# Performance work log

Measured on AMD Instinct MI355X. Metric: run time of the kernel, lower is better.

Reference implementation:

```python
import jax, jax.numpy as jnp
import numpy as np

S, N, IN = 4096, 32, 4
H, IF, SF, OUT = 64, 8, 4, 2
N_PAIRS = N * (N - 1)


def setup_inputs() -> dict:
    key = jax.random.key(0)
    ks = jax.random.split(key, 12)
    f = jax.random.normal
    return {
        "inputs": f(ks[0], (S, N, IN), jnp.float32),
        "L1W": f(ks[1], (H, IN), jnp.float32) * 0.1,
        "L1b": f(ks[2], (H,), jnp.float32) * 0.1,
        "L2W": f(ks[3], (H, H), jnp.float32) * 0.1,
        "L2b": f(ks[4], (H,), jnp.float32) * 0.1,
        "I1W": f(ks[5], (H, H), jnp.float32) * 0.1,
        "I2W": f(ks[6], (IF, H), jnp.float32) * 0.1,
        "I3": f(ks[7], (N_PAIRS, OUT, IF // OUT), jnp.float32) * 0.01,
        "S1W": f(ks[8], (SF, IN), jnp.float32) * 0.1,
        "S1b": f(ks[9], (SF,), jnp.float32) * 0.1,
        "S2W": f(ks[10], (N, OUT, SF // OUT), jnp.float32) * 0.01,
        "S2b": jnp.zeros((N, OUT), jnp.float32),
    }


def reference(inputs, L1W, L1b, L2W, L2b, I1W, I2W, I3, S1W, S1b, S2W, S2b):
    seq_len, n_obj = inputs.shape[:2]
    out_size = S2b.shape[1]

    # shared encoders (torch Linear: x @ W.T + b)
    h = jax.nn.relu(inputs @ L1W.T + L1b)
    h = jax.nn.relu(h @ L2W.T + L2b)          # [S, N, H]
    hs = jax.nn.relu(inputs @ S1W.T + S1b)    # [S, N, SF]

    # all pairwise differences Xi - Xj -> edge MLP (no biases)
    diff = h[:, :, None, :] - h[:, None, :, :]      # [S, N, N, H]
    pair = jnp.tanh(diff @ I1W.T)                   # [S, N, N, H]
    pair = jnp.tanh(pair @ I2W.T)                   # [S, N, N, IF]
    k_int = pair.shape[-1] // out_size
    pair = pair.reshape(seq_len, n_obj, n_obj, out_size, k_int)

    # scatter per-pair weights I3 into dense [N, N, OUT, k] using the
    # row-major Table ordering (i, j != i); diagonal stays zero, which
    # matches the original since diag pairwise features are exactly 0.
    ii, jj = np.nonzero(~np.eye(n_obj, dtype=bool))
    I3d = jnp.zeros((n_obj, n_obj, out_size, k_int), I3.dtype).at[ii, jj].set(I3)

    interaction = jnp.einsum('sijdk,ijdk->sid', pair, I3d)  # [S, N, OUT]

    k_self = hs.shape[-1] // out_size
    hs = hs.reshape(seq_len, n_obj, out_size, k_self)
    self_term = jnp.einsum('sidk,idk->sid', hs, S2W) + S2b  # [S, N, OUT]

    return interaction + self_term
```

## Files before the change

kernel.cpp:

```cpp
#include <hip/hip_runtime.h>
#include <math.h>

#define SEQ   4096
#define NOBJ  32
#define IN_F  4
#define HID   64
#define IFEAT 8
#define NPAIR_HALF 496

#define TWO_LOG2E 2.8853900817779268f

#if __has_builtin(__builtin_amdgcn_exp2f)
  #define EXP2F(x) __builtin_amdgcn_exp2f(x)
#else
  #define EXP2F(x) exp2f(x)
#endif

typedef _Float16 h2    __attribute__((ext_vector_type(2)));
typedef _Float16 f16x8 __attribute__((ext_vector_type(8)));
typedef float    f32x4 __attribute__((ext_vector_type(4)));

__device__ __forceinline__ h2 pack2(float a, float b) {
  return __builtin_bit_cast(h2, __builtin_amdgcn_cvt_pkrtz(a, b));
}
__device__ __forceinline__ unsigned pbits(h2 v) { return __builtin_bit_cast(unsigned, v); }

__device__ __forceinline__ f16x8 pack8(float4 a, float4 b) {
  int4 v;
  v.x = (int)pbits(pack2(a.x, a.y));
  v.y = (int)pbits(pack2(a.z, a.w));
  v.z = (int)pbits(pack2(b.x, b.y));
  v.w = (int)pbits(pack2(b.z, b.w));
  return __builtin_bit_cast(f16x8, v);
}

__device__ __forceinline__ float tanh_u(float x) {
  float e = EXP2F(x * TWO_LOG2E);
  float r = __builtin_amdgcn_rcpf(e + 1.0f);
  return fmaf(-2.0f, r, 1.0f);
}

__device__ __forceinline__ int pair_cum(int i) { return (i * (63 - i)) >> 1; }

__device__ __forceinline__ void pair_decode(int q, int& i, int& j) {
  int ii = (int)((63.0f - sqrtf(3969.0f - 8.0f * (float)q)) * 0.5f);
  if (ii > 0 && pair_cum(ii) > q) --ii;
  if (pair_cum(ii + 1) <= q)     ++ii;
  i = ii;
  j = ii + 1 + (q - pair_cum(ii));
}

__global__ __launch_bounds__(256, 4) void magnet_fused(
    const float* __restrict__ x,
    const float* __restrict__ L1W,
    const float* __restrict__ L1b,
    const float* __restrict__ L2W,
    const float* __restrict__ L2b,
    const float* __restrict__ I1W,
    const float* __restrict__ I2W,
    const float* __restrict__ I3,
    const float* __restrict__ S1W,
    const float* __restrict__ S1b,
    const float* __restrict__ S2W,
    const float* __restrict__ S2b,
    float* __restrict__ out)
{
  __shared__ __align__(16) float smem[6824];
  unsigned* sAtp   = (unsigned*)smem;
  unsigned* sBtp   = (unsigned*)(smem + 1152);
  float*    pairval = smem;
  float*    sE  = smem + 2304;
  float*    sEm = smem + 4480;
  float*    sx  = smem + 6656;
  float*    sW  = smem + 6784;

  const int t = threadIdx.x;
  const int s = blockIdx.x;

  if (t < NOBJ * IN_F) sx[t] = x[s * (NOBJ * IN_F) + t];
  if (t < IFEAT) {
    float a = 0.0f;
    const float4* w = (const float4*)(I2W + t * HID);
    #pragma unroll
    for (int c = 0; c < 16; ++c) { float4 v = w[c]; a += (v.x + v.y) + (v.z + v.w); }
    sW[t] = a;
  }
  __syncthreads();

  {
    const int n = t & 31, gI = t >> 5, kb = gI * 8;
    const float x0 = sx[n * 4 + 0], x1 = sx[n * 4 + 1];
    const float x2 = sx[n * 4 + 2], x3 = sx[n * 4 + 3];
    float a[8];
    #pragma unroll
    for (int r = 0; r < 8; ++r) {
      const int k = kb + r;
      const float4 w = *(const float4*)(L1W + k * 4);
      float v = L1b[k];
      v = fmaf(x0, w.x, v); v = fmaf(x1, w.y, v);
      v = fmaf(x2, w.z, v); v = fmaf(x3, w.w, v);
      a[r] = fmaxf(v, 0.0f);
    }
    int4 pk;
    pk.x = (int)pbits(pack2(a[0], a[1]));
    pk.y = (int)pbits(pack2(a[2], a[3]));
    pk.z = (int)pbits(pack2(a[4], a[5]));
    pk.w = (int)pbits(pack2(a[6], a[7]));
    *(int4*)(sAtp + n * 36 + gI * 4) = pk;
  }
  __syncthreads();

  const int lane = t & 63;
  const int wv   = t >> 6;
  const int qd   = lane >> 4;
  const int ln   = lane & 15;

  {
    const int m = 16 * wv + ln;
    const float* wr = L2W + m * HID;
    const f16x8 A0 = pack8(*(const float4*)(wr + 8 * qd),
                           *(const float4*)(wr + 8 * qd + 4));
    const f16x8 A1 = pack8(*(const float4*)(wr + 32 + 8 * qd),
                           *(const float4*)(wr + 32 + 8 * qd + 4));
    const float4 bias = *(const float4*)(L2b + 16 * wv + 4 * qd);
    #pragma unroll
    for (int nt = 0; nt < 2; ++nt) {
      const int n = nt * 16 + ln;
      const f16x8 B0 = __builtin_bit_cast(f16x8, *(const int4*)(sAtp + n * 36 + 4 * qd));
      const f16x8 B1 = __builtin_bit_cast(f16x8, *(const int4*)(sAtp + n * 36 + 16 + 4 * qd));
      f32x4 c; c[0] = bias.x; c[1] = bias.y; c[2] = bias.z; c[3] = bias.w;
      c = __builtin_amdgcn_mfma_f32_16x16x32_f16(A0, B0, c, 0, 0, 0);
      c = __builtin_amdgcn_mfma_f32_16x16x32_f16(A1, B1, c, 0, 0, 0);
      sBtp[n * 36 + 8 * wv + 2 * qd]     = pbits(pack2(fmaxf(c[0], 0.f), fmaxf(c[1], 0.f)));
      sBtp[n * 36 + 8 * wv + 2 * qd + 1] = pbits(pack2(fmaxf(c[2], 0.f), fmaxf(c[3], 0.f)));
    }
  }
  __syncthreads();

  {
    const int m = 16 * wv + ln;
    const float* wr = I1W + m * HID;
    const f16x8 A0 = pack8(*(const float4*)(wr + 8 * qd),
                           *(const float4*)(wr + 8 * qd + 4));
    const f16x8 A1 = pack8(*(const float4*)(wr + 32 + 8 * qd),
                           *(const float4*)(wr + 32 + 8 * qd + 4));
    #pragma unroll
    for (int nt = 0; nt < 2; ++nt) {
      const int n = nt * 16 + ln;
      const f16x8 B0 = __builtin_bit_cast(f16x8, *(const int4*)(sBtp + n * 36 + 4 * qd));
      const f16x8 B1 = __builtin_bit_cast(f16x8, *(const int4*)(sBtp + n * 36 + 16 + 4 * qd));
      f32x4 c; c[0] = 0.f; c[1] = 0.f; c[2] = 0.f; c[3] = 0.f;
      c = __builtin_amdgcn_mfma_f32_16x16x32_f16(A0, B0, c, 0, 0, 0);
      c = __builtin_amdgcn_mfma_f32_16x16x32_f16(A1, B1, c, 0, 0, 0);
      #pragma unroll
      for (int r = 0; r < 4; ++r) {
        const int mo = 16 * wv + 4 * qd + r;
        float gp = fminf(fmaxf(c[r] * TWO_LOG2E, -60.0f), 60.0f);
        sE [n * 68 + mo] = EXP2F(gp);
        sEm[n * 68 + mo] = EXP2F(-gp);
      }
    }
  }
  __syncthreads();

  {
    int i1, j1, i2, j2;
    pair_decode(t, i1, j1);
    const bool has2 = (t + 256) < NPAIR_HALF;
    pair_decode(has2 ? t + 256 : 0, i2, j2);

    float sWr[IFEAT];
    #pragma unroll
    for (int f = 0; f < IFEAT; ++f) sWr[f] = sW[f];

    float da[IFEAT] = {0.f,0.f,0.f,0.f,0.f,0.f,0.f,0.f};
    float db[IFEAT] = {0.f,0.f,0.f,0.f,0.f,0.f,0.f,0.f};
    const float4* Ei1 = (const float4*)(sE  + i1 * 68);
    const float4* Mj1 = (const float4*)(sEm + j1 * 68);
    const float4* Ei2 = (const float4*)(sE  + i2 * 68);
    const float4* Mj2 = (const float4*)(sEm + j2 * 68);

    #pragma unroll 4
    for (int hb = 0; hb < 16; ++hb) {
      const float4 a1 = Ei1[hb], b1 = Mj1[hb];
      const float4 a2 = Ei2[hb], b2 = Mj2[hb];
      float r1[4], r2[4];
      #pragma unroll
      for (int c = 0; c < 4; ++c) {
        r1[c] = __builtin_amdgcn_rcpf(fmaf((&a1.x)[c], (&b1.x)[c], 1.0f));
        r2[c] = __builtin_amdgcn_rcpf(fmaf((&a2.x)[c], (&b2.x)[c], 1.0f));
      }
      #pragma unroll
      for (int f = 0; f < IFEAT; ++f) {
        const float4 w = *(const float4*)(I2W + f * HID + hb * 4);
        da[f] = fmaf(w.x, r1[0], da[f]); da[f] = fmaf(w.y, r1[1], da[f]);
        da[f] = fmaf(w.z, r1[2], da[f]); da[f] = fmaf(w.w, r1[3], da[f]);
        db[f] = fmaf(w.x, r2[0], db[f]); db[f] = fmaf(w.y, r2[1], db[f]);
        db[f] = fmaf(w.z, r2[2], db[f]); db[f] = fmaf(w.w, r2[3], db[f]);
      }
    }

    {
      const float* cij = I3 + (i1 * 31 + (j1 - 1)) * 8;
      const float* cji = I3 + (j1 * 31 + i1) * 8;
      float vi0 = 0.f, vi1 = 0.f, vj0 = 0.f, vj1 = 0.f;
      #pragma unroll
      for (int k = 0; k < 4; ++k) {
        const float v = tanh_u(fmaf(-2.0f, da[k], sWr[k]));
        vi0 = fmaf(cij[k],  v, vi0);
        vj0 = fmaf(cji[k], -v, vj0);
      }
      #pragma unroll
      for (int k = 0; k < 4; ++k) {
        const float v = tanh_u(fmaf(-2.0f, da[4 + k], sWr[4 + k]));
        vi1 = fmaf(cij[4 + k],  v, vi1);
        vj1 = fmaf(cji[4 + k], -v, vj1);
      }
      float4 pv; pv.x = vi0; pv.y = vi1; pv.z = vj0; pv.w = vj1;
      *(float4*)(pairval + t * 4) = pv;
    }
    if (has2) {
      const float* cij = I3 + (i2 * 31 + (j2 - 1)) * 8;
      const float* cji = I3 + (j2 * 31 + i2) * 8;
      float vi0 = 0.f, vi1 = 0.f, vj0 = 0.f, vj1 = 0.f;
      #pragma unroll
      for (int k = 0; k < 4; ++k) {
        const float v = tanh_u(fmaf(-2.0f, db[k], sWr[k]));
        vi0 = fmaf(cij[k],  v, vi0);
        vj0 = fmaf(cji[k], -v, vj0);
      }
      #pragma unroll
      for (int k = 0; k < 4; ++k) {
        const float v = tanh_u(fmaf(-2.0f, db[4 + k], sWr[4 + k]));
        vi1 = fmaf(cij[4 + k],  v, vi1);
        vj1 = fmaf(cji[4 + k], -v, vj1);
      }
      float4 pv; pv.x = vi0; pv.y = vi1; pv.z = vj0; pv.w = vj1;
      *(float4*)(pairval + (t + 256) * 4) = pv;
    }
  }
  __syncthreads();

  if (t < 64) {
    const int i = t >> 1, d = t & 1;
    float sum = 0.0f;
    for (int j = 0; j < i; ++j)
      sum += pairval[(pair_cum(j) + (i - j - 1)) * 4 + 2 + d];
    const int base = pair_cum(i);
    for (int m = 0; m < 31 - i; ++m)
      sum += pairval[(base + m) * 4 + d];

    float res = S2b[t] + sum;
    #pragma unroll
    for (int k = 0; k < 2; ++k) {
      const int f = d * 2 + k;
      float hs = S1b[f];
      hs = fmaf(sx[i * 4 + 0], S1W[f * 4 + 0], hs);
      hs = fmaf(sx[i * 4 + 1], S1W[f * 4 + 1], hs);
      hs = fmaf(sx[i * 4 + 2], S1W[f * 4 + 2], hs);
      hs = fmaf(sx[i * 4 + 3], S1W[f * 4 + 3], hs);
      hs = fmaxf(hs, 0.0f);
      res = fmaf(hs, S2W[i * 4 + d * 2 + k], res);
    }
    out[s * (NOBJ * 2) + t] = res;
  }
}

extern "C" void kernel_launch(void* const* d_in, const int* in_sizes, int n_in,
                              void* d_out, int out_size, void* d_ws, size_t ws_size,
                              hipStream_t stream) {
  const float* x   = (const float*)d_in[0];
  const float* L1W = (const float*)d_in[1];
  const float* L1b = (const float*)d_in[2];
  const float* L2W = (const float*)d_in[3];
  const float* L2b = (const float*)d_in[4];
  const float* I1W = (const float*)d_in[5];
  const float* I2W = (const float*)d_in[6];
  const float* I3  = (const float*)d_in[7];
  const float* S1W = (const float*)d_in[8];
  const float* S1b = (const float*)d_in[9];
  const float* S2W = (const float*)d_in[10];
  const float* S2b = (const float*)d_in[11];
  float* outp = (float*)d_out;

  magnet_fused<<<SEQ, 256, 0, stream>>>(x, L1W, L1b, L2W, L2b, I1W, I2W, I3,
                                        S1W, S1b, S2W, S2b, outp);
}
```

Baseline: 130.1 us.

## Move pair second-layer projection onto MFMA and parallelize per-object reduction

Replaces the scalar per-thread FMA loop that projects the 64 reciprocal features of each pair onto the 8 edge outputs with 16x16x32 fp16 MFMA tiles, one tile of 16 pairs per wavefront iteration, with I2W staged once in LDS as packed halves. Pair tanh outputs are stored to LDS as fp16 and the I3 weighting moves to a new reduction stage, where all 256 threads each sum a quarter of an object's pairs before a final combine. This removes heavy scalar FMA work and repeated global I2W loads and spreads the serial 64-thread reduction over more threads. In exchange it adds fp16 rounding of the activations and intermediates, wastes MFMA columns because only 8 of 16 are used, and adds an extra barrier and scratch buffer.

After: 124.1 us. 4.6% less time.

```diff
diff --git a/kernel.cpp b/kernel.cpp
--- a/kernel.cpp
+++ b/kernel.cpp
@@ -7,6 +7,7 @@
 #define HID   64
 #define IFEAT 8
 #define NPAIR_HALF 496
+#define NTILE 31
 
 #define TWO_LOG2E 2.8853900817779268f
 
@@ -31,6 +32,15 @@
   v.y = (int)pbits(pack2(a.z, a.w));
   v.z = (int)pbits(pack2(b.x, b.y));
   v.w = (int)pbits(pack2(b.z, b.w));
+  return __builtin_bit_cast(f16x8, v);
+}
+
+__device__ __forceinline__ f16x8 pack8f(const float* r) {
+  int4 v;
+  v.x = (int)pbits(pack2(r[0], r[1]));
+  v.y = (int)pbits(pack2(r[2], r[3]));
+  v.z = (int)pbits(pack2(r[4], r[5]));
+  v.w = (int)pbits(pack2(r[6], r[7]));
   return __builtin_bit_cast(f16x8, v);
 }
 
@@ -65,14 +75,16 @@
     const float* __restrict__ S2b,
     float* __restrict__ out)
 {
-  __shared__ __align__(16) float smem[6824];
-  unsigned* sAtp   = (unsigned*)smem;
-  unsigned* sBtp   = (unsigned*)(smem + 1152);
-  float*    pairval = smem;
-  float*    sE  = smem + 2304;
-  float*    sEm = smem + 4480;
-  float*    sx  = smem + 6656;
-  float*    sW  = smem + 6784;
+  __shared__ __align__(16) float smem[7560];
+  unsigned*  sAtp = (unsigned*)smem;
+  unsigned*  sBtp = (unsigned*)(smem + 1152);
+  _Float16*  sv   = (_Float16*)smem;
+  float*     sE   = smem + 2304;
+  float*     sEm  = smem + 4480;
+  unsigned*  wB   = (unsigned*)(smem + 6656);
+  float*     sx   = smem + 7168;
+  float*     sW   = smem + 7296;
+  float*     part = smem + 7304;
 
   const int t = threadIdx.x;
   const int s = blockIdx.x;
@@ -84,6 +96,12 @@
     #pragma unroll
     for (int c = 0; c < 16; ++c) { float4 v = w[c]; a += (v.x + v.y) + (v.z + v.w); }
     sW[t] = a;
+  }
+  #pragma unroll
+  for (int idx = t; idx < 512; idx += 256) {
+    const int n = idx >> 5, k2 = idx & 31;
+    wB[idx] = (n < IFEAT)
+      ? pbits(pack2(I2W[n * HID + 2 * k2], I2W[n * HID + 2 * k2 + 1])) : 0u;
   }
   __syncthreads();
 
@@ -164,91 +182,73 @@
   __syncthreads();
 
   {
-    int i1, j1, i2, j2;
-    pair_decode(t, i1, j1);
-    const bool has2 = (t + 256) < NPAIR_HALF;
-    pair_decode(has2 ? t + 256 : 0, i2, j2);
-
-    float sWr[IFEAT];
-    #pragma unroll
-    for (int f = 0; f < IFEAT; ++f) sWr[f] = sW[f];
-
-    float da[IFEAT] = {0.f,0.f,0.f,0.f,0.f,0.f,0.f,0.f};
-    float db[IFEAT] = {0.f,0.f,0.f,0.f,0.f,0.f,0.f,0.f};
-    const float4* Ei1 = (const float4*)(sE  + i1 * 68);
-    const float4* Mj1 = (const float4*)(sEm + j1 * 68);
-    const float4* Ei2 = (const float4*)(sE  + i2 * 68);
-    const float4* Mj2 = (const float4*)(sEm + j2 * 68);
-
-    #pragma unroll 4
-    for (int hb = 0; hb < 16; ++hb) {
-      const float4 a1 = Ei1[hb], b1 = Mj1[hb];
-      const float4 a2 = Ei2[hb], b2 = Mj2[hb];
-      float r1[4], r2[4];
+    const f16x8 B0 = __builtin_bit_cast(f16x8, *(const int4*)(wB + ln * 32 + 4 * qd));
+    const f16x8 B1 = __builtin_bit_cast(f16x8, *(const int4*)(wB + ln * 32 + 16 + 4 * qd));
+    const float Wf = sW[ln & 7];
+
+    for (int tile = wv; tile < NTILE; tile += 4) {
+      int i, j;
+      pair_decode(tile * 16 + ln, i, j);
+      const float* Ei = sE  + i * 68 + qd * 8;
+      const float* Mj = sEm + j * 68 + qd * 8;
+      const float4 e0 = *(const float4*)(Ei);
+      const float4 e1 = *(const float4*)(Ei + 4);
+      const float4 e2 = *(const float4*)(Ei + 32);
+      const float4 e3 = *(const float4*)(Ei + 36);
+      const float4 m0 = *(const float4*)(Mj);
+      const float4 m1 = *(const float4*)(Mj + 4);
+      const float4 m2 = *(const float4*)(Mj + 32);
+      const float4 m3 = *(const float4*)(Mj + 36);
+      float r0[8], r1[8];
       #pragma unroll
       for (int c = 0; c < 4; ++c) {
-        r1[c] = __builtin_amdgcn_rcpf(fmaf((&a1.x)[c], (&b1.x)[c], 1.0f));
-        r2[c] = __builtin_amdgcn_rcpf(fmaf((&a2.x)[c], (&b2.x)[c], 1.0f));
+        r0[c]     = __builtin_amdgcn_rcpf(fmaf((&e0.x)[c], (&m0.x)[c], 1.0f));
+        r0[4 + c] = __builtin_amdgcn_rcpf(fmaf((&e1.x)[c], (&m1.x)[c], 1.0f));
+        r1[c]     = __builtin_amdgcn_rcpf(fmaf((&e2.x)[c], (&m2.x)[c], 1.0f));
+        r1[4 + c] = __builtin_amdgcn_rcpf(fmaf((&e3.x)[c], (&m3.x)[c], 1.0f));
       }
-      #pragma unroll
-      for (int f = 0; f < IFEAT; ++f) {
-        const float4 w = *(const float4*)(I2W + f * HID + hb * 4);
-        da[f] = fmaf(w.x, r1[0], da[f]); da[f] = fmaf(w.y, r1[1], da[f]);
-        da[f] = fmaf(w.z, r1[2], da[f]); da[f] = fmaf(w.w, r1[3], da[f]);
-        db[f] = fmaf(w.x, r2[0], db[f]); db[f] = fmaf(w.y, r2[1], db[f]);
-        db[f] = fmaf(w.z, r2[2], db[f]); db[f] = fmaf(w.w, r2[3], db[f]);
+      const f16x8 A0 = pack8f(r0);
+      const f16x8 A1 = pack8f(r1);
+      f32x4 c; c[0] = 0.f; c[1] = 0.f; c[2] = 0.f; c[3] = 0.f;
+      c = __builtin_amdgcn_mfma_f32_16x16x32_f16(A0, B0, c, 0, 0, 0);
+      c = __builtin_amdgcn_mfma_f32_16x16x32_f16(A1, B1, c, 0, 0, 0);
+      if (ln < IFEAT) {
+        #pragma unroll
+        for (int r = 0; r < 4; ++r) {
+          const float v = tanh_u(fmaf(-2.0f, c[r], Wf));
+          sv[(tile * 16 + 4 * qd + r) * 8 + ln] = (_Float16)v;
+        }
       }
     }
-
-    {
-      const float* cij = I3 + (i1 * 31 + (j1 - 1)) * 8;
-      const float* cji = I3 + (j1 * 31 + i1) * 8;
-      float vi0 = 0.f, vi1 = 0.f, vj0 = 0.f, vj1 = 0.f;
-      #pragma unroll
-      for (int k = 0; k < 4; ++k) {
-        const float v = tanh_u(fmaf(-2.0f, da[k], sWr[k]));
-        vi0 = fmaf(cij[k],  v, vi0);
-        vj0 = fmaf(cji[k], -v, vj0);
-      }
-      #pragma unroll
-      for (int k = 0; k < 4; ++k) {
-        const float v = tanh_u(fmaf(-2.0f, da[4 + k], sWr[4 + k]));
-        vi1 = fmaf(cij[4 + k],  v, vi1);
-        vj1 = fmaf(cji[4 + k], -v, vj1);
-      }
-      float4 pv; pv.x = vi0; pv.y = vi1; pv.z = vj0; pv.w = vj1;
-      *(float4*)(pairval + t * 4) = pv;
-    }
-    if (has2) {
-      const float* cij = I3 + (i2 * 31 + (j2 - 1)) * 8;
-      const float* cji = I3 + (j2 * 31 + i2) * 8;
-      float vi0 = 0.f, vi1 = 0.f, vj0 = 0.f, vj1 = 0.f;
-      #pragma unroll
-      for (int k = 0; k < 4; ++k) {
-        const float v = tanh_u(fmaf(-2.0f, db[k], sWr[k]));
-        vi0 = fmaf(cij[k],  v, vi0);
-        vj0 = fmaf(cji[k], -v, vj0);
-      }
-      #pragma unroll
-      for (int k = 0; k < 4; ++k) {
-        const float v = tanh_u(fmaf(-2.0f, db[4 + k], sWr[4 + k]));
-        vi1 = fmaf(cij[4 + k],  v, vi1);
-        vj1 = fmaf(cji[4 + k], -v, vj1);
-      }
-      float4 pv; pv.x = vi0; pv.y = vi1; pv.z = vj0; pv.w = vj1;
-      *(float4*)(pairval + (t + 256) * 4) = pv;
-    }
+  }
+  __syncthreads();
+
+  {
+    const int i = t >> 3, d = (t >> 2) & 1, qtr = t & 3;
+    const int mend = (qtr == 3) ? 31 : (qtr * 8 + 8);
+    float sum = 0.0f;
+    for (int m = qtr * 8; m < mend; ++m) {
+      const int j = m + (m >= i);
+      int q, row; float sgn;
+      if (j > i) { q = pair_cum(i) + (j - i - 1); row = i * 31 + j - 1; sgn =  1.0f; }
+      else       { q = pair_cum(j) + (i - j - 1); row = i * 31 + j;     sgn = -1.0f; }
+      const h2* vp = (const h2*)(sv + q * 8 + d * 4);
+      const h2 va = vp[0], vb = vp[1];
+      const float4 cf = *(const float4*)(I3 + row * 8 + d * 4);
+      float dot;
+      dot = cf.x * (float)va.x;
+      dot = fmaf(cf.y, (float)va.y, dot);
+      dot = fmaf(cf.z, (float)vb.x, dot);
+      dot = fmaf(cf.w, (float)vb.y, dot);
+      sum = fmaf(sgn, dot, sum);
+    }
+    part[t] = sum;
   }
   __syncthreads();
 
   if (t < 64) {
     const int i = t >> 1, d = t & 1;
-    float sum = 0.0f;
-    for (int j = 0; j < i; ++j)
-      sum += pairval[(pair_cum(j) + (i - j - 1)) * 4 + 2 + d];
-    const int base = pair_cum(i);
-    for (int m = 0; m < 31 - i; ++m)
-      sum += pairval[(base + m) * 4 + d];
+    float sum = part[t * 4] + part[t * 4 + 1] + part[t * 4 + 2] + part[t * 4 + 3];
 
     float res = S2b[t] + sum;
     #pragma unroll
```
